# Performance work log

Hardware: AMD Instinct MI355X
Metric: run time of the kernel (lower is better)

## Reference

```python
import jax, jax.numpy as jnp
import numpy as np

EMBED_DIM = 1024
N_HEADS = 16
HEAD_DIM = EMBED_DIM // N_HEADS


def setup_inputs() -> dict:
    key = jax.random.key(0)
    ks = jax.random.split(key, 6)
    B, S, D = 4, 2048, EMBED_DIM
    s = 1.0 / np.sqrt(D)
    return {
        "x": jax.random.normal(ks[0], (B, S, D), dtype=jnp.float32),
        "Wq": jax.random.normal(ks[1], (D, D), dtype=jnp.float32) * s,
        "Wk": jax.random.normal(ks[2], (D, D), dtype=jnp.float32) * s,
        "Wv": jax.random.normal(ks[3], (D, D), dtype=jnp.float32) * s,
        "Wo": jax.random.normal(ks[4], (D, D), dtype=jnp.float32) * s,
        "bo": jax.random.normal(ks[5], (D,), dtype=jnp.float32) * 0.01,
    }


def reference(x, Wq, Wk, Wv, Wo, bo):
    B, S, D = x.shape
    H, Hd = N_HEADS, HEAD_DIM
    # q,k,v: [B,S,D] -> [B,H,S,Hd]
    def proj(W):
        return (x @ W.T).reshape(B, S, H, Hd).transpose(0, 2, 1, 3)
    q, k, v = proj(Wq), proj(Wk), proj(Wv)
    scores = jnp.einsum("bhqd,bhkd->bhqk", q, k) / jnp.sqrt(jnp.float32(Hd))
    attn = jax.nn.softmax(scores, axis=-1)  # dropout p=0.0 -> identity
    out = jnp.einsum("bhqk,bhkd->bhqd", attn, v)  # [B,H,S,Hd]
    out = out.transpose(0, 2, 1, 3).reshape(B, S, D)
    return out @ Wo.T + bo
```

## Files before the change

kernel.cpp:

```cpp
#include <hip/hip_runtime.h>


typedef unsigned short u16;
typedef unsigned int u32;
typedef float f32x4 __attribute__((ext_vector_type(4)));
typedef float f32x16 __attribute__((ext_vector_type(16)));
typedef short s16x8 __attribute__((ext_vector_type(8)));

#define DEVI __device__ __forceinline__

DEVI u16 f32_bf16(float f) {
  unsigned u = __float_as_uint(f);
  return (u16)((u + 0x7FFFu + ((u >> 16) & 1u)) >> 16);
}

DEVI u32 pack_pk(float a, float b) {
  u32 r;
  asm("v_cvt_pk_bf16_f32 %0, %1, %2" : "=v"(r) : "v"(a), "v"(b));
  return r;
}

DEVI void gload_lds16(const void* g, void* l) {
  __builtin_amdgcn_global_load_lds((const __attribute__((address_space(1))) void*)g,
                                   (__attribute__((address_space(3))) void*)l, 16, 0, 0);
}

#if __has_builtin(__builtin_amdgcn_permlane32_swap)
typedef int i32x2 __attribute__((ext_vector_type(2)));
DEVI void plswap(u32& a, u32& b, int hi) {
  i32x2 r = __builtin_amdgcn_permlane32_swap((int)a, (int)b, false, false);
  a = (u32)r[0];
  b = (u32)r[1];
}
#else
DEVI void plswap(u32& a, u32& b, int hi) {
  u32 ta = (u32)__shfl_xor((int)a, 32);
  u32 tb = (u32)__shfl_xor((int)b, 32);
  u32 na = hi ? tb : a;
  u32 nb = hi ? b : ta;
  a = na;
  b = nb;
}
#endif

__global__ void cvt_kernel(const float* __restrict__ in, u16* __restrict__ out, int n4) {
  int i = blockIdx.x * 256 + threadIdx.x;
  if (i >= n4) return;
  float4 v = ((const float4*)in)[i];
  ushort4 o;
  o.x = f32_bf16(v.x); o.y = f32_bf16(v.y);
  o.z = f32_bf16(v.z); o.w = f32_bf16(v.w);
  ((ushort4*)out)[i] = o;
}

__global__ void cvt_w_kernel(const float* __restrict__ wq, const float* __restrict__ wk,
                             const float* __restrict__ wv, const float* __restrict__ wo,
                             u16* __restrict__ wcat, u16* __restrict__ wo_bf) {
  int i = blockIdx.x * 256 + threadIdx.x;
  int m = blockIdx.y;
  const float* src = (m == 0) ? wq : (m == 1) ? wk : (m == 2) ? wv : wo;
  u16* dst = (m < 3) ? (wcat + m * 1048576) : wo_bf;
  float4 v = ((const float4*)src)[i];
  ushort4 o;
  o.x = f32_bf16(v.x); o.y = f32_bf16(v.y);
  o.z = f32_bf16(v.z); o.w = f32_bf16(v.w);
  ((ushort4*)dst)[i] = o;
}

template <int MODE>
__global__ __launch_bounds__(256, 2) void gemm_bt(
    const u16* __restrict__ A, const u16* __restrict__ B, void* __restrict__ Cout,
    const float* __restrict__ bias, int M, int N, int K) {
  __shared__ u16 As[128 * 32];
  __shared__ u16 Bs[128 * 32];
  const int tid = threadIdx.x;
  const int lane = tid & 63;
  const int w = tid >> 6;
  const int wr = w >> 1, wc = w & 1;
  const int l15 = lane & 15, l4 = lane >> 4;

  const int gx = gridDim.x;
  const int nwg = gx * gridDim.y;
  int i = blockIdx.y * gx + blockIdx.x;
  int t = (i & 7) * (nwg >> 3) + (i >> 3);
  const int m0 = (t / gx) * 128, n0 = (t % gx) * 128;

  f32x4 acc[4][4] = {};

  for (int k0 = 0; k0 < K; k0 += 32) {
    __syncthreads();
#pragma unroll
    for (int i2 = 0; i2 < 2; ++i2) {
      int cb = i2 * 256 + w * 64;
      int c = cb + lane;
      gload_lds16(A + (m0 + (c >> 2)) * K + k0 + (c & 3) * 8, &As[cb * 8]);
      gload_lds16(B + (n0 + (c >> 2)) * K + k0 + (c & 3) * 8, &Bs[cb * 8]);
    }
    __syncthreads();

    s16x8 af[4], bf[4];
#pragma unroll
    for (int m = 0; m < 4; ++m)
      af[m] = *(const s16x8*)&As[(wr * 64 + m * 16 + l15) * 32 + l4 * 8];
#pragma unroll
    for (int n = 0; n < 4; ++n)
      bf[n] = *(const s16x8*)&Bs[(wc * 64 + n * 16 + l15) * 32 + l4 * 8];
#pragma unroll
    for (int m = 0; m < 4; ++m)
#pragma unroll
      for (int n = 0; n < 4; ++n)
        acc[m][n] = __builtin_amdgcn_mfma_f32_16x16x32_bf16(af[m], bf[n], acc[m][n], 0, 0, 0);
  }

#pragma unroll
  for (int m = 0; m < 4; ++m) {
    int row = m0 + wr * 64 + m * 16 + l4 * 4;
#pragma unroll
    for (int n = 0; n < 4; ++n) {
      int col = n0 + wc * 64 + n * 16 + l15;
      if (MODE == 0) {
        u16* C = (u16*)Cout;
        float scale = (col < 1024) ? 0.18033688f : 1.0f;
#pragma unroll
        for (int j = 0; j < 4; ++j)
          C[(row + j) * N + col] = f32_bf16(acc[m][n][j] * scale);
      } else {
        float* C = (float*)Cout;
        float bb = bias[col];
#pragma unroll
        for (int j = 0; j < 4; ++j)
          C[(row + j) * N + col] = acc[m][n][j] + bb;
      }
    }
  }
}

__global__ __launch_bounds__(256, 2) void attn_kernel(const u16* __restrict__ QKV,
                                                      u16* __restrict__ AO) {
  __shared__ u16 Ks[2][64 * 64];
  __shared__ u16 Vt[2][64 * 64];
  const int tid = threadIdx.x;
  const int lane = tid & 63, w = tid >> 6;
  const int l31 = lane & 31, hi = lane >> 5;

  int ib = blockIdx.z * 256 + blockIdx.y * 16 + blockIdx.x;
  int tb = (ib & 7) * 128 + (ib >> 3);
  const int h = (tb >> 4) & 15, b = tb >> 8;
  const int rowbase = b * 2048;
  const int q0 = (tb & 15) * 128 + w * 32;

  s16x8 qa[4];
  {
    const u16* qp = QKV + (size_t)(rowbase + q0 + l31) * 3072 + h * 64 + hi * 8;
#pragma unroll
    for (int s = 0; s < 4; ++s) qa[s] = *(const s16x8*)(qp + s * 16);
  }

  const char* kbase = (const char*)(QKV + (size_t)rowbase * 3072 + 1024 + h * 64);
  const u16* vbase = QKV + (size_t)rowbase * 3072 + 2048 + h * 64;

  const int kgrow = lane >> 3;
  const int kgcol = ((lane & 7) * 16) ^ ((lane >> 3) << 4);
  const int kv = (tid & 31) * 2;
  const int dv = (tid >> 5) * 8;

  f32x16 o0 = {}, o1 = {};
  float mrow = -1e30f, lrow = 0.f;

  {
#pragma unroll
    for (int c = 0; c < 2; ++c) {
      int chunk = w * 2 + c;
      gload_lds16(kbase + (chunk * 8 + kgrow) * 6144 + kgcol, &Ks[0][chunk * 512]);
    }
    const u16* vp = vbase + kv * 3072 + dv;
    s16x8 v0 = *(const s16x8*)vp, v1 = *(const s16x8*)(vp + 3072);
#pragma unroll
    for (int i = 0; i < 8; ++i) {
      int d = dv + i;
      *(u32*)((char*)&Vt[0][0] + d * 128 + ((kv * 2) ^ ((d & 7) << 4))) =
          (u32)(u16)v0[i] | ((u32)(u16)v1[i] << 16);
    }
  }
  __syncthreads();

  for (int kt = 0; kt < 32; ++kt) {
    const int cur = kt & 1;
    s16x8 v0, v1;
    if (kt < 31) {
      const char* kb = kbase + (size_t)(kt + 1) * 64 * 6144;
#pragma unroll
      for (int c = 0; c < 2; ++c) {
        int chunk = w * 2 + c;
        gload_lds16(kb + (chunk * 8 + kgrow) * 6144 + kgcol, &Ks[cur ^ 1][chunk * 512]);
      }
      const u16* vp = vbase + ((kt + 1) * 64 + kv) * 3072 + dv;
      v0 = *(const s16x8*)vp;
      v1 = *(const s16x8*)(vp + 3072);
    }

    const char* Kb = (const char*)&Ks[cur][0];
    const char* Vb = (const char*)&Vt[cur][0];

    f32x16 sacc[2];
#pragma unroll
    for (int step = 0; step < 2; ++step) {
      const int keyrow = step * 32 + l31;
      const int swzk = (keyrow & 7) << 4;
      f32x16 t = {};
      __builtin_amdgcn_s_setprio(1);
#pragma unroll
      for (int s = 0; s < 4; ++s) {
        s16x8 kf = *(const s16x8*)(Kb + keyrow * 128 + ((s * 32 + hi * 16) ^ swzk));
        t = __builtin_amdgcn_mfma_f32_32x32x16_bf16(kf, qa[s], t, 0, 0, 0);
      }
      __builtin_amdgcn_s_setprio(0);
      sacc[step] = t;
    }

#pragma unroll
    for (int step = 0; step < 2; ++step) {
      f32x16 s_acc = sacc[step];
      float mx[8];
#pragma unroll
      for (int r = 0; r < 8; ++r) mx[r] = fmaxf(s_acc[r], s_acc[r + 8]);
#pragma unroll
      for (int r = 0; r < 4; ++r) mx[r] = fmaxf(mx[r], mx[r + 4]);
      float m4 = fmaxf(fmaxf(mx[0], mx[1]), fmaxf(mx[2], mx[3]));
      m4 = fmaxf(m4, __shfl_xor(m4, 32));
      if (!__all(m4 <= mrow + 8.f)) {
        float mnew = fmaxf(mrow, m4);
        float corr = __builtin_amdgcn_exp2f(mrow - mnew);
        lrow *= corr;
#pragma unroll
        for (int r = 0; r < 16; ++r) { o0[r] *= corr; o1[r] *= corr; }
        mrow = mnew;
      }
      float p[16];
#pragma unroll
      for (int r = 0; r < 16; ++r) p[r] = __builtin_amdgcn_exp2f(s_acc[r] - mrow);
      float sm[8];
#pragma unroll
      for (int r = 0; r < 8; ++r) sm[r] = p[r] + p[r + 8];
#pragma unroll
      for (int r = 0; r < 4; ++r) sm[r] += sm[r + 4];
      float rs = (sm[0] + sm[1]) + (sm[2] + sm[3]);
      rs += __shfl_xor(rs, 32);
      lrow += rs;

      u32 pk[8];
#pragma unroll
      for (int j = 0; j < 8; ++j) pk[j] = pack_pk(p[2 * j], p[2 * j + 1]);
      plswap(pk[0], pk[2], hi);
      plswap(pk[1], pk[3], hi);
      plswap(pk[4], pk[6], hi);
      plswap(pk[5], pk[7], hi);
      union { u32 u[4]; s16x8 v; } pb0, pb1;
      pb0.u[0] = pk[0]; pb0.u[1] = pk[1]; pb0.u[2] = pk[2]; pb0.u[3] = pk[3];
      pb1.u[0] = pk[4]; pb1.u[1] = pk[5]; pb1.u[2] = pk[6]; pb1.u[3] = pk[7];

      const int swzv = (l31 & 7) << 4;
      __builtin_amdgcn_s_setprio(1);
#pragma unroll
      for (int ks = 0; ks < 2; ++ks) {
        int cbyte = (step * 64 + ks * 32 + hi * 16) ^ swzv;
        s16x8 vf0 = *(const s16x8*)(Vb + l31 * 128 + cbyte);
        s16x8 vf1 = *(const s16x8*)(Vb + (32 + l31) * 128 + cbyte);
        s16x8 pf = ks ? pb1.v : pb0.v;
        o0 = __builtin_amdgcn_mfma_f32_32x32x16_bf16(vf0, pf, o0, 0, 0, 0);
        o1 = __builtin_amdgcn_mfma_f32_32x32x16_bf16(vf1, pf, o1, 0, 0, 0);
      }
      __builtin_amdgcn_s_setprio(0);
    }

    if (kt < 31) {
#pragma unroll
      for (int i = 0; i < 8; ++i) {
        int d = dv + i;
        *(u32*)((char*)&Vt[cur ^ 1][0] + d * 128 + ((kv * 2) ^ ((d & 7) << 4))) =
            (u32)(u16)v0[i] | ((u32)(u16)v1[i] << 16);
      }
    }
    __syncthreads();
  }

  float inv = __builtin_amdgcn_rcpf(lrow);
  u16* op = AO + (size_t)(rowbase + q0 + l31) * 1024 + h * 64;
#pragma unroll
  for (int g = 0; g < 4; ++g) {
    ushort4 s0, s1;
    s0.x = f32_bf16(o0[g * 4 + 0] * inv);
    s0.y = f32_bf16(o0[g * 4 + 1] * inv);
    s0.z = f32_bf16(o0[g * 4 + 2] * inv);
    s0.w = f32_bf16(o0[g * 4 + 3] * inv);
    s1.x = f32_bf16(o1[g * 4 + 0] * inv);
    s1.y = f32_bf16(o1[g * 4 + 1] * inv);
    s1.z = f32_bf16(o1[g * 4 + 2] * inv);
    s1.w = f32_bf16(o1[g * 4 + 3] * inv);
    *(ushort4*)(op + g * 8 + 4 * hi) = s0;
    *(ushort4*)(op + 32 + g * 8 + 4 * hi) = s1;
  }
}

extern "C" void kernel_launch(void* const* d_in, const int* in_sizes, int n_in,
                              void* d_out, int out_size, void* d_ws, size_t ws_size,
                              hipStream_t stream) {
  const float* x = (const float*)d_in[0];
  const float* Wq = (const float*)d_in[1];
  const float* Wk = (const float*)d_in[2];
  const float* Wv = (const float*)d_in[3];
  const float* Wo = (const float*)d_in[4];
  const float* bo = (const float*)d_in[5];
  float* out = (float*)d_out;

  char* ws = (char*)d_ws;
  u16* x_bf = (u16*)ws;
  u16* Wcat = (u16*)(ws + 16777216);
  u16* Wo_bf = (u16*)(ws + 16777216 + 6291456);
  u16* QKV = (u16*)(ws + 16777216 + 6291456 + 2097152);
  u16* AO = (u16*)(ws + 16777216 + 6291456 + 2097152 + 50331648);

  cvt_kernel<<<8192, 256, 0, stream>>>(x, x_bf, 8192 * 1024 / 4);
  cvt_w_kernel<<<dim3(1024, 4), 256, 0, stream>>>(Wq, Wk, Wv, Wo, Wcat, Wo_bf);

  gemm_bt<0><<<dim3(24, 64), 256, 0, stream>>>(x_bf, Wcat, QKV, nullptr, 8192, 3072, 1024);
  attn_kernel<<<dim3(16, 16, 4), 256, 0, stream>>>(QKV, AO);
  gemm_bt<1><<<dim3(8, 64), 256, 0, stream>>>(AO, Wo_bf, out, bo, 8192, 1024, 1024);
}
```

Before: 212.4 us.

## Replace GEMM with 256x256-tile double-buffered swizzled-LDS pipelined kernel

Replaces the 128x128, K=32 single-buffered GEMM with a 512-thread 256x256 tile kernel using K=64 steps, double-buffered LDS, and XOR-swizzled LDS layout. Global-to-LDS loads for the next K tile are issued in stages interleaved with MFMA work, guarded by explicit vmcnt waits and barriers, with setprio around MFMA bursts. The aim is to hide memory latency, raise data reuse per tile, and avoid LDS bank conflicts. In exchange it uses 128KB of LDS per block and launches fewer blocks (384 and 128), which may leave CUs underused, especially for the output projection.

```diff
diff --git a/kernel.cpp b/kernel.cpp
--- a/kernel.cpp
+++ b/kernel.cpp
@@ -68,68 +68,129 @@
 }
 
 template <int MODE>
-__global__ __launch_bounds__(256, 2) void gemm_bt(
+__global__ __launch_bounds__(512, 2) void gemm256(
     const u16* __restrict__ A, const u16* __restrict__ B, void* __restrict__ Cout,
     const float* __restrict__ bias, int M, int N, int K) {
-  __shared__ u16 As[128 * 32];
-  __shared__ u16 Bs[128 * 32];
+  __shared__ u16 SA[2][256 * 64];
+  __shared__ u16 SB[2][256 * 64];
   const int tid = threadIdx.x;
-  const int lane = tid & 63;
-  const int w = tid >> 6;
-  const int wr = w >> 1, wc = w & 1;
+  const int lane = tid & 63, w = tid >> 6;
+  const int wm = w >> 2, wn = w & 3;
   const int l15 = lane & 15, l4 = lane >> 4;
+  const int swz = (l15 & 7) << 3;
 
   const int gx = gridDim.x;
   const int nwg = gx * gridDim.y;
-  int i = blockIdx.y * gx + blockIdx.x;
-  int t = (i & 7) * (nwg >> 3) + (i >> 3);
-  const int m0 = (t / gx) * 128, n0 = (t % gx) * 128;
-
-  f32x4 acc[4][4] = {};
-
-  for (int k0 = 0; k0 < K; k0 += 32) {
-    __syncthreads();
-#pragma unroll
-    for (int i2 = 0; i2 < 2; ++i2) {
-      int cb = i2 * 256 + w * 64;
-      int c = cb + lane;
-      gload_lds16(A + (m0 + (c >> 2)) * K + k0 + (c & 3) * 8, &As[cb * 8]);
-      gload_lds16(B + (n0 + (c >> 2)) * K + k0 + (c & 3) * 8, &Bs[cb * 8]);
-    }
-    __syncthreads();
-
-    s16x8 af[4], bf[4];
-#pragma unroll
-    for (int m = 0; m < 4; ++m)
-      af[m] = *(const s16x8*)&As[(wr * 64 + m * 16 + l15) * 32 + l4 * 8];
-#pragma unroll
-    for (int n = 0; n < 4; ++n)
-      bf[n] = *(const s16x8*)&Bs[(wc * 64 + n * 16 + l15) * 32 + l4 * 8];
-#pragma unroll
-    for (int m = 0; m < 4; ++m)
-#pragma unroll
-      for (int n = 0; n < 4; ++n)
-        acc[m][n] = __builtin_amdgcn_mfma_f32_16x16x32_bf16(af[m], bf[n], acc[m][n], 0, 0, 0);
-  }
-
-#pragma unroll
-  for (int m = 0; m < 4; ++m) {
-    int row = m0 + wr * 64 + m * 16 + l4 * 4;
-#pragma unroll
-    for (int n = 0; n < 4; ++n) {
-      int col = n0 + wc * 64 + n * 16 + l15;
+  int ib = blockIdx.y * gx + blockIdx.x;
+  int t = (ib & 7) * (nwg >> 3) + (ib >> 3);
+  const int m0 = (t / gx) * 256, n0 = (t % gx) * 256;
+
+  const int srow = w * 8 + (lane >> 3);
+  const int scol = ((lane & 7) ^ (lane >> 3)) * 8;
+
+  const u16* Ab = A + (size_t)m0 * K;
+  const u16* Bb = B + (size_t)n0 * K;
+
+  f32x4 acc[8][4] = {};
+
+  gload_lds16(Bb + (size_t)(0 * 64 + srow) * K + scol, &SB[0][0 * 4096 + w * 512]);
+  gload_lds16(Bb + (size_t)(1 * 64 + srow) * K + scol, &SB[0][1 * 4096 + w * 512]);
+  gload_lds16(Bb + (size_t)(2 * 64 + srow) * K + scol, &SB[0][2 * 4096 + w * 512]);
+  gload_lds16(Bb + (size_t)(3 * 64 + srow) * K + scol, &SB[0][3 * 4096 + w * 512]);
+  gload_lds16(Ab + (size_t)(0 * 64 + srow) * K + scol, &SA[0][0 * 4096 + w * 512]);
+  gload_lds16(Ab + (size_t)(2 * 64 + srow) * K + scol, &SA[0][2 * 4096 + w * 512]);
+  gload_lds16(Ab + (size_t)(1 * 64 + srow) * K + scol, &SA[0][1 * 4096 + w * 512]);
+  gload_lds16(Ab + (size_t)(3 * 64 + srow) * K + scol, &SA[0][3 * 4096 + w * 512]);
+
+  const int NT = K >> 6;
+  for (int tt = 0; tt < NT; ++tt) {
+    const int p = tt & 1;
+    const u16* sa = &SA[p][0];
+    const u16* sb = &SB[p][0];
+    u16* na = &SA[p ^ 1][0];
+    u16* nb = &SB[p ^ 1][0];
+    const int kn = (tt + 1) << 6;
+    const bool more = (tt + 1) < NT;
+
+    s16x8 bf[4][2];
+#pragma unroll
+    for (int q = 0; q < 4; ++q) {
+      if (q == 0) {
+        asm volatile("s_waitcnt vmcnt(2)" ::: "memory");
+        __builtin_amdgcn_s_barrier();
+        __builtin_amdgcn_sched_barrier(0);
+        if (more) {
+          gload_lds16(Bb + (size_t)(0 * 64 + srow) * K + kn + scol, &nb[0 * 4096 + w * 512]);
+          gload_lds16(Bb + (size_t)(1 * 64 + srow) * K + kn + scol, &nb[1 * 4096 + w * 512]);
+        }
+#pragma unroll
+        for (int nf = 0; nf < 4; ++nf)
+#pragma unroll
+          for (int ks = 0; ks < 2; ++ks)
+            bf[nf][ks] = *(const s16x8*)&sb[(wn * 64 + nf * 16 + l15) * 64 +
+                                            ((ks * 32 + l4 * 8) ^ swz)];
+      } else if (q == 1) {
+        if (more) {
+          gload_lds16(Bb + (size_t)(2 * 64 + srow) * K + kn + scol, &nb[2 * 4096 + w * 512]);
+          gload_lds16(Bb + (size_t)(3 * 64 + srow) * K + kn + scol, &nb[3 * 4096 + w * 512]);
+        }
+      } else if (q == 2) {
+        if (more) {
+          asm volatile("s_waitcnt vmcnt(4)" ::: "memory");
+        } else {
+          asm volatile("s_waitcnt vmcnt(0)" ::: "memory");
+        }
+        __builtin_amdgcn_s_barrier();
+        __builtin_amdgcn_sched_barrier(0);
+        if (more) {
+          gload_lds16(Ab + (size_t)(0 * 64 + srow) * K + kn + scol, &na[0 * 4096 + w * 512]);
+          gload_lds16(Ab + (size_t)(2 * 64 + srow) * K + kn + scol, &na[2 * 4096 + w * 512]);
+        }
+      } else {
+        if (more) {
+          gload_lds16(Ab + (size_t)(1 * 64 + srow) * K + kn + scol, &na[1 * 4096 + w * 512]);
+          gload_lds16(Ab + (size_t)(3 * 64 + srow) * K + kn + scol, &na[3 * 4096 + w * 512]);
+        }
+      }
+
+      s16x8 af[2][2];
+#pragma unroll
+      for (int m2 = 0; m2 < 2; ++m2)
+#pragma unroll
+        for (int ks = 0; ks < 2; ++ks)
+          af[m2][ks] = *(const s16x8*)&sa[(wm * 128 + (q * 2 + m2) * 16 + l15) * 64 +
+                                          ((ks * 32 + l4 * 8) ^ swz)];
+      __builtin_amdgcn_s_setprio(1);
+#pragma unroll
+      for (int m2 = 0; m2 < 2; ++m2)
+#pragma unroll
+        for (int nf = 0; nf < 4; ++nf)
+#pragma unroll
+          for (int ks = 0; ks < 2; ++ks)
+            acc[q * 2 + m2][nf] = __builtin_amdgcn_mfma_f32_16x16x32_bf16(
+                af[m2][ks], bf[nf][ks], acc[q * 2 + m2][nf], 0, 0, 0);
+      __builtin_amdgcn_s_setprio(0);
+    }
+  }
+
+#pragma unroll
+  for (int mf = 0; mf < 8; ++mf) {
+    int row = m0 + wm * 128 + mf * 16 + l4 * 4;
+#pragma unroll
+    for (int nf = 0; nf < 4; ++nf) {
+      int col = n0 + wn * 64 + nf * 16 + l15;
       if (MODE == 0) {
         u16* C = (u16*)Cout;
         float scale = (col < 1024) ? 0.18033688f : 1.0f;
 #pragma unroll
         for (int j = 0; j < 4; ++j)
-          C[(row + j) * N + col] = f32_bf16(acc[m][n][j] * scale);
+          C[(size_t)(row + j) * N + col] = f32_bf16(acc[mf][nf][j] * scale);
       } else {
         float* C = (float*)Cout;
         float bb = bias[col];
 #pragma unroll
         for (int j = 0; j < 4; ++j)
-          C[(row + j) * N + col] = acc[m][n][j] + bb;
+          C[(size_t)(row + j) * N + col] = acc[mf][nf][j] + bb;
       }
     }
   }
@@ -323,7 +384,7 @@
   cvt_kernel<<<8192, 256, 0, stream>>>(x, x_bf, 8192 * 1024 / 4);
   cvt_w_kernel<<<dim3(1024, 4), 256, 0, stream>>>(Wq, Wk, Wv, Wo, Wcat, Wo_bf);
 
-  gemm_bt<0><<<dim3(24, 64), 256, 0, stream>>>(x_bf, Wcat, QKV, nullptr, 8192, 3072, 1024);
+  gemm256<0><<<dim3(12, 32), 512, 0, stream>>>(x_bf, Wcat, QKV, nullptr, 8192, 3072, 1024);
   attn_kernel<<<dim3(16, 16, 4), 256, 0, stream>>>(QKV, AO);
-  gemm_bt<1><<<dim3(8, 64), 256, 0, stream>>>(AO, Wo_bf, out, bo, 8192, 1024, 1024);
-}
+  gemm256<1><<<dim3(4, 32), 512, 0, stream>>>(AO, Wo_bf, out, bo, 8192, 1024, 1024);
+}
```

Result: slower. 250.0 us (+17.7%).

## Double GEMM K-tile to 64 with XOR-swizzled LDS and raise occupancy bounds

Applied to the files above, without the earlier changes.

The bf16 GEMM now stages a 64-wide K slice per iteration instead of 32, which halves the barrier count per unit of work. LDS writes and reads use an XOR swizzle on the column index to avoid bank conflicts on the wider rows. MFMA issue is wrapped in s_setprio, and launch bounds rise to 3 waves per EU for the GEMM and 4 for attention. The larger LDS tiles and higher occupancy targets may force register spills or limit how many blocks are actually resident.

```diff
diff --git a/kernel.cpp b/kernel.cpp
--- a/kernel.cpp
+++ b/kernel.cpp
@@ -68,48 +68,63 @@
 }
 
 template <int MODE>
-__global__ __launch_bounds__(256, 2) void gemm_bt(
+__global__ __launch_bounds__(256, 3) void gemm_bt(
     const u16* __restrict__ A, const u16* __restrict__ B, void* __restrict__ Cout,
     const float* __restrict__ bias, int M, int N, int K) {
-  __shared__ u16 As[128 * 32];
-  __shared__ u16 Bs[128 * 32];
+  __shared__ u16 As[128 * 64];
+  __shared__ u16 Bs[128 * 64];
   const int tid = threadIdx.x;
   const int lane = tid & 63;
   const int w = tid >> 6;
   const int wr = w >> 1, wc = w & 1;
   const int l15 = lane & 15, l4 = lane >> 4;
+  const int swz = (l15 & 7) << 3;
 
   const int gx = gridDim.x;
   const int nwg = gx * gridDim.y;
-  int i = blockIdx.y * gx + blockIdx.x;
-  int t = (i & 7) * (nwg >> 3) + (i >> 3);
+  int ib = blockIdx.y * gx + blockIdx.x;
+  int t = (ib & 7) * (nwg >> 3) + (ib >> 3);
   const int m0 = (t / gx) * 128, n0 = (t % gx) * 128;
 
+  const int srow = w * 8 + (lane >> 3);
+  const int scol = ((lane & 7) ^ (lane >> 3)) * 8;
+
   f32x4 acc[4][4] = {};
 
-  for (int k0 = 0; k0 < K; k0 += 32) {
+  for (int k0 = 0; k0 < K; k0 += 64) {
     __syncthreads();
 #pragma unroll
-    for (int i2 = 0; i2 < 2; ++i2) {
-      int cb = i2 * 256 + w * 64;
-      int c = cb + lane;
-      gload_lds16(A + (m0 + (c >> 2)) * K + k0 + (c & 3) * 8, &As[cb * 8]);
-      gload_lds16(B + (n0 + (c >> 2)) * K + k0 + (c & 3) * 8, &Bs[cb * 8]);
+    for (int i = 0; i < 4; ++i) {
+      int cb = i * 256 + w * 64;
+      int r = i * 32 + srow;
+      gload_lds16(A + (size_t)(m0 + r) * K + k0 + scol, &As[cb * 8]);
+      gload_lds16(B + (size_t)(n0 + r) * K + k0 + scol, &Bs[cb * 8]);
     }
     __syncthreads();
 
-    s16x8 af[4], bf[4];
+    s16x8 af[4][2], bf[4][2];
 #pragma unroll
     for (int m = 0; m < 4; ++m)
-      af[m] = *(const s16x8*)&As[(wr * 64 + m * 16 + l15) * 32 + l4 * 8];
+#pragma unroll
+      for (int ks = 0; ks < 2; ++ks)
+        af[m][ks] = *(const s16x8*)&As[(wr * 64 + m * 16 + l15) * 64 +
+                                       ((ks * 32 + l4 * 8) ^ swz)];
 #pragma unroll
     for (int n = 0; n < 4; ++n)
-      bf[n] = *(const s16x8*)&Bs[(wc * 64 + n * 16 + l15) * 32 + l4 * 8];
+#pragma unroll
+      for (int ks = 0; ks < 2; ++ks)
+        bf[n][ks] = *(const s16x8*)&Bs[(wc * 64 + n * 16 + l15) * 64 +
+                                       ((ks * 32 + l4 * 8) ^ swz)];
+    __builtin_amdgcn_s_setprio(1);
 #pragma unroll
     for (int m = 0; m < 4; ++m)
 #pragma unroll
       for (int n = 0; n < 4; ++n)
-        acc[m][n] = __builtin_amdgcn_mfma_f32_16x16x32_bf16(af[m], bf[n], acc[m][n], 0, 0, 0);
+#pragma unroll
+        for (int ks = 0; ks < 2; ++ks)
+          acc[m][n] = __builtin_amdgcn_mfma_f32_16x16x32_bf16(af[m][ks], bf[n][ks],
+                                                              acc[m][n], 0, 0, 0);
+    __builtin_amdgcn_s_setprio(0);
   }
 
 #pragma unroll
@@ -123,19 +138,19 @@
         float scale = (col < 1024) ? 0.18033688f : 1.0f;
 #pragma unroll
         for (int j = 0; j < 4; ++j)
-          C[(row + j) * N + col] = f32_bf16(acc[m][n][j] * scale);
+          C[(size_t)(row + j) * N + col] = f32_bf16(acc[m][n][j] * scale);
       } else {
         float* C = (float*)Cout;
         float bb = bias[col];
 #pragma unroll
         for (int j = 0; j < 4; ++j)
-          C[(row + j) * N + col] = acc[m][n][j] + bb;
-      }
-    }
-  }
-}
-
-__global__ __launch_bounds__(256, 2) void attn_kernel(const u16* __restrict__ QKV,
+          C[(size_t)(row + j) * N + col] = acc[m][n][j] + bb;
+      }
+    }
+  }
+}
+
+__global__ __launch_bounds__(256, 4) void attn_kernel(const u16* __restrict__ QKV,
                                                       u16* __restrict__ AO) {
   __shared__ u16 Ks[2][64 * 64];
   __shared__ u16 Vt[2][64 * 64];
```

Result: faster. 202.4 us (-4.7%).
